# Performance work log

Hardware: AMD Instinct MI355X
Metric: run time of the kernel (lower is better)

Reference implementation:

```python
import jax, jax.numpy as jnp
import numpy as np

B, S, D, H = 4, 2048, 2048, 16
DK = D // H

def setup_inputs() -> dict:
    key = jax.random.key(0)
    ks = jax.random.split(key, 9)
    def xavier(k, shape):
        fan_in, fan_out = shape[1], shape[0]
        limit = (6.0 / (fan_in + fan_out)) ** 0.5
        return jax.random.uniform(k, shape, jnp.float32, -limit, limit)
    return {
        "x": jax.random.normal(ks[0], (B, S, D), jnp.float32),
        "Wq": xavier(ks[1], (D, D)), "bq": jnp.zeros((D,), jnp.float32),
        "Wk": xavier(ks[2], (D, D)), "bk": jnp.zeros((D,), jnp.float32),
        "Wv": xavier(ks[3], (D, D)), "bv": jnp.zeros((D,), jnp.float32),
        "Wo": xavier(ks[4], (D, D)), "bo": jnp.zeros((D,), jnp.float32),
    }

def reference(x, Wq, bq, Wk, bk, Wv, bv, Wo, bo):
    b, s, d = x.shape
    scale = DK ** 0.5
    # torch nn.Linear: y = x @ W.T + b
    def proj(W, bias):
        y = jnp.einsum('bsd,ed->bse', x, W) + bias
        return y.reshape(b, s, H, DK).transpose(0, 2, 1, 3)  # (b, h, s, dk)
    Q, K, V = proj(Wq, bq), proj(Wk, bk), proj(Wv, bv)
    scores = jnp.einsum('bhqd,bhkd->bhqk', Q, K) / scale
    causal = jnp.triu(jnp.ones((s, s), dtype=bool), k=1)
    scores = jnp.where(causal[None, None], -jnp.inf, scores)
    attn = jax.nn.softmax(scores, axis=-1)
    ctx = jnp.einsum('bhqk,bhkd->bhqd', attn, V)
    ctx = ctx.transpose(0, 2, 1, 3).reshape(b, s, d)
    out = jnp.einsum('bsd,ed->bse', ctx, Wo) + bo
    return out
```

## Files before the change

kernel.cpp:

```cpp
#include <hip/hip_runtime.h>
#include <hip/hip_bf16.h>
#include <cstdint>

#define B_  4
#define S_  2048
#define D_  2048
#define H_  16
#define DK_ 128

typedef __attribute__((ext_vector_type(8))) short short8;
typedef __attribute__((ext_vector_type(4))) short s16x4;
typedef __attribute__((ext_vector_type(4))) float f32x4;
typedef unsigned short ushort_t;

__device__ __forceinline__ void gl_lds16(const void* g, void* l) {
  __builtin_amdgcn_global_load_lds(
      (const __attribute__((address_space(1))) uint32_t*)g,
      (__attribute__((address_space(3))) uint32_t*)l, 16, 0, 0);
}

__device__ __forceinline__ ushort_t f2bf(float f) {
  __hip_bfloat16 h = __float2bfloat16(f);
  return *(ushort_t*)&h;
}

__global__ __launch_bounds__(256) void cvt_all(
    const float* __restrict__ x,  const float* __restrict__ w0,
    const float* __restrict__ w1, const float* __restrict__ w2,
    const float* __restrict__ w3, ushort_t* __restrict__ dst)
{
  constexpr size_t NE = (size_t)B_ * S_ * D_;
  constexpr size_t NW = (size_t)D_ * D_;
  constexpr int XB = (int)(NE / 8 / 256);
  constexpr int WB = (int)(NW / 8 / 256);

  const int blk = blockIdx.x;
  const float* src;
  size_t base;
  int li;
  if (blk < XB)           { src = x;  base = 0;           li = blk * 256 + threadIdx.x; }
  else if (blk < XB+WB)   { src = w0; base = NE/8;        li = (blk-XB)     * 256 + threadIdx.x; }
  else if (blk < XB+2*WB) { src = w1; base = (NE+NW)/8;   li = (blk-XB-WB)  * 256 + threadIdx.x; }
  else if (blk < XB+3*WB) { src = w2; base = (NE+2*NW)/8; li = (blk-XB-2*WB)* 256 + threadIdx.x; }
  else                    { src = w3; base = (NE+3*NW)/8; li = (blk-XB-3*WB)* 256 + threadIdx.x; }

  float4 a = ((const float4*)src)[li * 2];
  float4 b = ((const float4*)src)[li * 2 + 1];
  short8 o;
  o[0] = (short)f2bf(a.x); o[1] = (short)f2bf(a.y);
  o[2] = (short)f2bf(a.z); o[3] = (short)f2bf(a.w);
  o[4] = (short)f2bf(b.x); o[5] = (short)f2bf(b.y);
  o[6] = (short)f2bf(b.z); o[7] = (short)f2bf(b.w);
  ((short8*)dst)[base + li] = o;
}

#define STAGE_A(d, q, tt) do {                                             \
    int r0_ = (q) * 64 + w * 8;                                            \
    gl_lds16(Agb + (size_t)(r0_ + lr) * 2048 + (tt) * 64 + lc, &As[d][r0_ * 64]); \
    r0_ += 128;                                                            \
    gl_lds16(Agb + (size_t)(r0_ + lr) * 2048 + (tt) * 64 + lc, &As[d][r0_ * 64]); \
  } while (0)
#define STAGE_B(d, q, tt) do {                                             \
    int r0_ = (w >> 1) * 64 + (q) * 32 + ((w & 1) * 2) * 8;                \
    gl_lds16(Wgb + (size_t)(r0_ + lr) * 2048 + (tt) * 64 + lc, &Bs[d][r0_ * 64]); \
    r0_ += 8;                                                              \
    gl_lds16(Wgb + (size_t)(r0_ + lr) * 2048 + (tt) * 64 + lc, &Bs[d][r0_ * 64]); \
  } while (0)

#define LDA_Q(d, qm) do {                                                  \
    _Pragma("unroll")                                                      \
    for (int fm = 0; fm < 4; ++fm)                                         \
      _Pragma("unroll")                                                    \
      for (int kk = 0; kk < 2; ++kk) {                                     \
        const int row = wm * 128 + (qm) * 64 + fm * 16 + l15;              \
        aA[fm][kk] = *(const short8*)&As[d][row * 64 + (((kk * 4 + lhi) ^ (l15 & 7)) << 3)]; \
      }                                                                    \
  } while (0)

#define LDB_Q(d, bi, qn) do {                                              \
    _Pragma("unroll")                                                      \
    for (int fn = 0; fn < 2; ++fn)                                         \
      _Pragma("unroll")                                                    \
      for (int kk = 0; kk < 2; ++kk) {                                     \
        const int row = wn * 64 + (qn) * 32 + fn * 16 + l15;               \
        bB[bi][fn][kk] = *(const short8*)&Bs[d][row * 64 + (((kk * 4 + lhi) ^ (l15 & 7)) << 3)]; \
      }                                                                    \
  } while (0)

#define MM_Q(am, bi) do {                                                  \
    __builtin_amdgcn_s_setprio(1);                                         \
    _Pragma("unroll")                                                      \
    for (int kk = 0; kk < 2; ++kk)                                         \
      _Pragma("unroll")                                                    \
      for (int fm = 0; fm < 4; ++fm)                                       \
        _Pragma("unroll")                                                  \
        for (int fn = 0; fn < 2; ++fn)                                     \
          acc[(am) * 4 + fm][(bi) * 2 + fn] = __builtin_amdgcn_mfma_f32_16x16x32_bf16( \
              aA[fm][kk], bB[bi][fn][kk], acc[(am) * 4 + fm][(bi) * 2 + fn], 0, 0, 0); \
    __builtin_amdgcn_s_setprio(0);                                         \
  } while (0)

#define GEMM_BODY()                                                        \
  f32x4 acc[8][4] = {};                                                    \
  short8 aA[4][2];                                                         \
  short8 bB[2][2][2];                                                      \
        \
  STAGE_A(0, 0, 0); STAGE_B(0, 0, 0); STAGE_B(0, 1, 0); STAGE_A(0, 1, 0);  \
  STAGE_A(1, 0, 1); STAGE_B(1, 0, 1); STAGE_B(1, 1, 1);                    \
  asm volatile("s_waitcnt vmcnt(6)" ::: "memory");                         \
  __builtin_amdgcn_s_barrier();                                            \
  for (int j = 0; j < NJ; ++j) {                                           \
    const int u = 2 * j;                                                   \
    const bool stg = (j + 1 < NJ);                                         \
                      \
    LDA_Q(0, 0); LDB_Q(0, 0, 0);                                           \
    STAGE_A(1, 1, u + 1);                                                  \
    __builtin_amdgcn_s_barrier();                                          \
    MM_Q(0, 0);                                                            \
    __builtin_amdgcn_s_barrier();                                          \
                                            \
    LDB_Q(0, 1, 1);                                                        \
    if (stg) STAGE_A(0, 0, u + 2);                                         \
    __builtin_amdgcn_s_barrier();                                          \
    MM_Q(0, 1);                                                            \
    __builtin_amdgcn_s_barrier();                                          \
                                            \
    LDA_Q(0, 1);                                                           \
    if (stg) STAGE_B(0, 0, u + 2);                                         \
    __builtin_amdgcn_s_barrier();                                          \
    MM_Q(1, 0);                                                            \
    __builtin_amdgcn_s_barrier();                                          \
                                            \
    if (stg) STAGE_B(0, 1, u + 2);                                         \
    __builtin_amdgcn_s_barrier();                                          \
    MM_Q(1, 1);                                                            \
    if (stg) { asm volatile("s_waitcnt vmcnt(6)" ::: "memory"); }          \
    else     { asm volatile("s_waitcnt vmcnt(0)" ::: "memory"); }          \
    __builtin_amdgcn_s_barrier();                                          \
                                \
    LDA_Q(1, 0); LDB_Q(1, 0, 0);                                           \
    if (stg) STAGE_A(0, 1, u + 2);                                         \
    __builtin_amdgcn_s_barrier();                                          \
    MM_Q(0, 0);                                                            \
    __builtin_amdgcn_s_barrier();                                          \
                                            \
    LDB_Q(1, 1, 1);                                                        \
    if (stg) STAGE_A(1, 0, u + 3);                                         \
    __builtin_amdgcn_s_barrier();                                          \
    MM_Q(0, 1);                                                            \
    __builtin_amdgcn_s_barrier();                                          \
                                            \
    LDA_Q(1, 1);                                                           \
    if (stg) STAGE_B(1, 0, u + 3);                                         \
    __builtin_amdgcn_s_barrier();                                          \
    MM_Q(1, 0);                                                            \
    __builtin_amdgcn_s_barrier();                                          \
                                            \
    if (stg) STAGE_B(1, 1, u + 3);                                         \
    __builtin_amdgcn_s_barrier();                                          \
    MM_Q(1, 1);                                                            \
    if (stg) { asm volatile("s_waitcnt vmcnt(6)" ::: "memory"); }          \
    __builtin_amdgcn_s_barrier();                                          \
  }

__global__ __launch_bounds__(512, 2) void gemmQKV(
    const ushort_t* __restrict__ A,
    const ushort_t* __restrict__ Wqm, const ushort_t* __restrict__ Wkm,
    const ushort_t* __restrict__ Wvm,
    const float* __restrict__ bq, const float* __restrict__ bk,
    const float* __restrict__ bv,
    ushort_t* __restrict__ Qo, ushort_t* __restrict__ Ko,
    ushort_t* __restrict__ Vo)
{
  constexpr int NJ = (D_ / 64) / 2;

  __shared__ ushort_t As[2][256 * 64];
  __shared__ ushort_t Bs[2][256 * 64];

  const int bid = blockIdx.x;
  const int c = bid & 7;
  const int j0 = bid >> 3;
  const int proj = j0 >> 5;
  const int s = j0 & 31;
  const int tnl = s & 7;
  const int tm = c * 4 + (s >> 3);

  const ushort_t* Wsel = (proj == 0) ? Wqm : (proj == 1) ? Wkm : Wvm;
  const float*    bsel = (proj == 0) ? bq  : (proj == 1) ? bk  : bv;
  ushort_t*       osel = (proj == 0) ? Qo  : (proj == 1) ? Ko  : Vo;

  const int t = threadIdx.x;
  const int l = t & 63;
  const int w = t >> 6;
  const int wm = w >> 2;
  const int wn = w & 3;
  const int l15 = l & 15, lhi = l >> 4;
  const int lr = l >> 3;
  const int lc = ((l & 7) ^ lr) * 8;

  const ushort_t* Agb = A + (size_t)(tm * 256) * 2048;
  const ushort_t* Wgb = Wsel + (size_t)(tnl * 256) * 2048;

  GEMM_BODY()

#pragma unroll
  for (int qn = 0; qn < 2; ++qn)
#pragma unroll
    for (int fn = 0; fn < 2; ++fn) {
      const int e = tnl * 256 + wn * 64 + qn * 32 + fn * 16 + l15;
      const float bvv = bsel[e];
      const int h = e >> 7, dk = e & (DK_ - 1);
#pragma unroll
      for (int qm = 0; qm < 2; ++qm)
#pragma unroll
        for (int fm = 0; fm < 4; ++fm) {
          const int srow0 = tm * 256 + wm * 128 + qm * 64 + fm * 16 + lhi * 4;
          const f32x4 v4 = acc[qm * 4 + fm][qn * 2 + fn];
          if (proj == 2) {
            const int b = srow0 >> 11, s0 = srow0 & (S_ - 1);
            s16x4 pk;
#pragma unroll
            for (int r = 0; r < 4; ++r) pk[r] = (short)f2bf(v4[r] + bvv);
            *(s16x4*)(osel + (((size_t)b * H_ + h) * DK_ + dk) * S_ + s0) = pk;
          } else {
#pragma unroll
            for (int r = 0; r < 4; ++r) {
              const int sg = srow0 + r;
              const int b = sg >> 11, sR = sg & (S_ - 1);
              osel[(((size_t)b * H_ + h) * S_ + sR) * DK_ + dk] = f2bf(v4[r] + bvv);
            }
          }
        }
    }
}

__global__ __launch_bounds__(512, 2) void gemmOut(
    const ushort_t* __restrict__ A,
    const ushort_t* __restrict__ W,
    const float* __restrict__ bias,
    float* __restrict__ outp)
{
  constexpr int NJ = (D_ / 64) / 2;
  constexpr int NWG = (B_ * S_ / 256) * (D_ / 256);

  __shared__ ushort_t As[2][256 * 64];
  __shared__ ushort_t Bs[2][256 * 64];

  const int bid = blockIdx.x;
  const int swz = (bid & 7) * (NWG / 8) + (bid >> 3);
  const int tm = swz >> 3;
  const int tn = swz & 7;

  const int t = threadIdx.x;
  const int l = t & 63;
  const int w = t >> 6;
  const int wm = w >> 2;
  const int wn = w & 3;
  const int l15 = l & 15, lhi = l >> 4;
  const int lr = l >> 3;
  const int lc = ((l & 7) ^ lr) * 8;

  const ushort_t* Agb = A + (size_t)(tm * 256) * 2048;
  const ushort_t* Wgb = W + (size_t)(tn * 256) * 2048;

  GEMM_BODY()

#pragma unroll
  for (int qn = 0; qn < 2; ++qn)
#pragma unroll
    for (int fn = 0; fn < 2; ++fn) {
      const int e = tn * 256 + wn * 64 + qn * 32 + fn * 16 + l15;
      const float bvv = bias[e];
#pragma unroll
      for (int qm = 0; qm < 2; ++qm)
#pragma unroll
        for (int fm = 0; fm < 4; ++fm) {
          const int srow0 = tm * 256 + wm * 128 + qm * 64 + fm * 16 + lhi * 4;
          const f32x4 v4 = acc[qm * 4 + fm][qn * 2 + fn];
#pragma unroll
          for (int r = 0; r < 4; ++r)
            outp[(size_t)(srow0 + r) * D_ + e] = v4[r] + bvv;
        }
    }
}
#undef STAGE_A
#undef STAGE_B
#undef LDA_Q
#undef LDB_Q
#undef MM_Q
#undef GEMM_BODY

__global__ __launch_bounds__(256, 2) void attn_kern(
    const ushort_t* __restrict__ Q,
    const ushort_t* __restrict__ K,
    const ushort_t* __restrict__ Vt,
    ushort_t* __restrict__ C)
{
  __shared__ ushort_t Ks[2][64 * 128];
  __shared__ ushort_t Vs[2][128 * 64];
  __shared__ ushort_t Pl[4][32 * 64];

  const int bid = blockIdx.x;
  const int i = bid >> 3;
  const int bh = (bid & 7) * 8 + (i >> 3);
  const int qp = i & 7;

  const ushort_t* Qg = Q + (size_t)bh * S_ * DK_;
  const ushort_t* Kg = K + (size_t)bh * S_ * DK_;
  const ushort_t* Vg = Vt + (size_t)bh * DK_ * S_;
  const int b = bh >> 4, h = bh & 15;

  const int t = threadIdx.x;
  const int l = t & 63;
  const int w = t >> 6;
  const int l15 = l & 15, lhi = l >> 4;

  const float cs = 0.08838834764831845f * 1.4426950408889634f;
  const float DEFER_RAW = 8.0f / cs;

  short8 ones;
#pragma unroll
  for (int j = 0; j < 8; ++j) ones[j] = (short)0x3F80;

  int koff[4], voff[4];
#pragma unroll
  for (int j = 0; j < 4; ++j) {
    const int krow = w * 16 + j * 4 + lhi;
    koff[j] = krow * DK_ + 8 * (l15 ^ ((j * 4 + lhi) & 7));
    const int vrow = (w * 4 + j) * 8 + (l >> 3);
    voff[j] = vrow * S_ + 8 * ((l & 7) ^ (l >> 3));
  }
  int kcol[4];
#pragma unroll
  for (int kt = 0; kt < 4; ++kt)
    kcol[kt] = ((kt * 64 + lhi * 16) ^ ((l15 & 7) << 4)) >> 1;
  int vcol[2];
#pragma unroll
  for (int hb = 0; hb < 2; ++hb)
    vcol[hb] = ((hb * 64 + lhi * 16) ^ ((l15 & 7) << 4)) >> 1;

#define STAGE_KV(pb, kvv) do {                                              \
    _Pragma("unroll")                                                       \
    for (int j = 0; j < 4; ++j) {                                           \
      gl_lds16(Kg + (size_t)(kvv) * DK_ + koff[j], Ks[pb] + (w * 4 + j) * 512); \
      gl_lds16(Vg + (size_t)(kvv) + voff[j],       Vs[pb] + (w * 4 + j) * 512); \
    }                                                                       \
  } while (0)

  for (int pass = 0; pass < 2; ++pass) {
    const int qb = pass ? (15 - qp) : qp;
    const int qrow0 = qb * 128 + w * 32;
    const int nkv = 2 * (qb + 1);

    short8 qa[2][4];
#pragma unroll
    for (int rf = 0; rf < 2; ++rf)
#pragma unroll
      for (int kt = 0; kt < 4; ++kt)
        qa[rf][kt] = *(const short8*)(Qg + (size_t)(qrow0 + rf * 16 + l15) * DK_ + kt * 32 + lhi * 8);

    f32x4 o[2][8] = {};
    f32x4 lsum[2] = {};
    float mrow[2][4];
#pragma unroll
    for (int rf = 0; rf < 2; ++rf)
#pragma unroll
      for (int r = 0; r < 4; ++r) mrow[rf][r] = -1e30f;

    STAGE_KV(0, 0);
    asm volatile("s_waitcnt vmcnt(0)" ::: "memory");
    __syncthreads();

    for (int kvt = 0; kvt < nkv; ++kvt) {
      const int kv = kvt * 64;
      const int p = kvt & 1;

      if (kvt + 1 < nkv) STAGE_KV(p ^ 1, kv + 64);

      f32x4 sf[2][4] = {};
      __builtin_amdgcn_s_setprio(1);
#pragma unroll
      for (int f = 0; f < 4; ++f) {
#pragma unroll
        for (int kt = 0; kt < 4; ++kt) {
          short8 kb = *(const short8*)(Ks[p] + (f * 16 + l15) * 128 + kcol[kt]);
          sf[0][f] = __builtin_amdgcn_mfma_f32_16x16x32_bf16(qa[0][kt], kb, sf[0][f], 0, 0, 0);
          sf[1][f] = __builtin_amdgcn_mfma_f32_16x16x32_bf16(qa[1][kt], kb, sf[1][f], 0, 0, 0);
        }
      }
      __builtin_amdgcn_s_setprio(0);

      float pmax[2][4];
#pragma unroll
      for (int rf = 0; rf < 2; ++rf)
#pragma unroll
        for (int r = 0; r < 4; ++r) pmax[rf][r] = -1e30f;
      const bool domask = (kv + 63 > qrow0);
      if (domask) {
#pragma unroll
        for (int f = 0; f < 4; ++f) {
          const int col = kv + f * 16 + l15;
#pragma unroll
          for (int rf = 0; rf < 2; ++rf)
#pragma unroll
            for (int r = 0; r < 4; ++r) {
              const int row = qrow0 + rf * 16 + lhi * 4 + r;
              if (col > row) sf[rf][f][r] = -1e30f;
              pmax[rf][r] = fmaxf(pmax[rf][r], sf[rf][f][r]);
            }
        }
      } else {
#pragma unroll
        for (int f = 0; f < 4; ++f)
#pragma unroll
          for (int rf = 0; rf < 2; ++rf)
#pragma unroll
            for (int r = 0; r < 4; ++r)
              pmax[rf][r] = fmaxf(pmax[rf][r], sf[rf][f][r]);
      }
#pragma unroll
      for (int d = 1; d < 16; d <<= 1)
#pragma unroll
        for (int rf = 0; rf < 2; ++rf)
#pragma unroll
          for (int r = 0; r < 4; ++r)
            pmax[rf][r] = fmaxf(pmax[rf][r], __shfl_xor(pmax[rf][r], d, 64));

      bool need = false;
#pragma unroll
      for (int rf = 0; rf < 2; ++rf)
#pragma unroll
        for (int r = 0; r < 4; ++r) need |= (pmax[rf][r] > mrow[rf][r] + DEFER_RAW);
      if (__any(need)) {
#pragma unroll
        for (int rf = 0; rf < 2; ++rf)
#pragma unroll
          for (int r = 0; r < 4; ++r) {
            const float mn = fmaxf(mrow[rf][r], pmax[rf][r]);
            const float alpha = __builtin_amdgcn_exp2f((mrow[rf][r] - mn) * cs);
            mrow[rf][r] = mn;
            lsum[rf][r] *= alpha;
#pragma unroll
            for (int n = 0; n < 8; ++n) o[rf][n][r] *= alpha;
          }
      }

      ushort_t* P = Pl[w];
#pragma unroll
      for (int f = 0; f < 4; ++f)
#pragma unroll
        for (int rf = 0; rf < 2; ++rf)
#pragma unroll
          for (int r = 0; r < 4; ++r) {
            const float pv = __builtin_amdgcn_exp2f((sf[rf][f][r] - mrow[rf][r]) * cs);
            const int prow = rf * 16 + lhi * 4 + r;
            P[prow * 64 + ((f * 16 + l15) ^ ((prow & 7) << 3))] = f2bf(pv);
          }

      asm volatile("s_waitcnt lgkmcnt(0)" ::: "memory");
      short8 pa[2][2];
#pragma unroll
      for (int rf = 0; rf < 2; ++rf)
#pragma unroll
        for (int ks = 0; ks < 2; ++ks) {
          const int prow = rf * 16 + l15;
          pa[rf][ks] = *(const short8*)(P + prow * 64 + ((ks * 32 + lhi * 8) ^ ((prow & 7) << 3)));
        }

      __builtin_amdgcn_s_setprio(1);
#pragma unroll
      for (int rf = 0; rf < 2; ++rf) {
        lsum[rf] = __builtin_amdgcn_mfma_f32_16x16x32_bf16(pa[rf][0], ones, lsum[rf], 0, 0, 0);
        lsum[rf] = __builtin_amdgcn_mfma_f32_16x16x32_bf16(pa[rf][1], ones, lsum[rf], 0, 0, 0);
      }
#pragma unroll
      for (int n = 0; n < 8; ++n) {
#pragma unroll
        for (int hb = 0; hb < 2; ++hb) {
          short8 vb = *(const short8*)(Vs[p] + (n * 16 + l15) * 64 + vcol[hb]);
          o[0][n] = __builtin_amdgcn_mfma_f32_16x16x32_bf16(pa[0][hb], vb, o[0][n], 0, 0, 0);
          o[1][n] = __builtin_amdgcn_mfma_f32_16x16x32_bf16(pa[1][hb], vb, o[1][n], 0, 0, 0);
        }
      }
      __builtin_amdgcn_s_setprio(0);

      asm volatile("s_waitcnt vmcnt(0)" ::: "memory");
      __syncthreads();
    }

#pragma unroll
    for (int rf = 0; rf < 2; ++rf) {
      float linv[4];
#pragma unroll
      for (int r = 0; r < 4; ++r) linv[r] = 1.0f / lsum[rf][r];
#pragma unroll
      for (int n = 0; n < 8; ++n) {
        const int dk = n * 16 + l15;
#pragma unroll
        for (int r = 0; r < 4; ++r) {
          const int srow = qrow0 + rf * 16 + lhi * 4 + r;
          C[(((size_t)b * S_ + srow) * H_ + h) * DK_ + dk] = f2bf(o[rf][n][r] * linv[r]);
        }
      }
    }
  }
#undef STAGE_KV
}

extern "C" void kernel_launch(void* const* d_in, const int* in_sizes, int n_in,
                              void* d_out, int out_size, void* d_ws, size_t ws_size,
                              hipStream_t stream) {
  const float* x  = (const float*)d_in[0];
  const float* Wq = (const float*)d_in[1];
  const float* bq = (const float*)d_in[2];
  const float* Wk = (const float*)d_in[3];
  const float* bk = (const float*)d_in[4];
  const float* Wv = (const float*)d_in[5];
  const float* bv = (const float*)d_in[6];
  const float* Wo = (const float*)d_in[7];
  const float* bo = (const float*)d_in[8];
  float* out = (float*)d_out;

  ushort_t* ws = (ushort_t*)d_ws;
  const size_t NE = (size_t)B_ * S_ * D_;
  const size_t NW = (size_t)D_ * D_;
  ushort_t* xb  = ws;
  ushort_t* Wqb = ws + NE;
  ushort_t* Wkb = Wqb + NW;
  ushort_t* Wvb = Wkb + NW;
  ushort_t* Wob = Wvb + NW;
  ushort_t* Qw  = Wob + NW;
  ushort_t* Kw  = Qw + NE;
  ushort_t* Vw  = Kw + NE;
  ushort_t* Cw  = xb;

  const int XB = (int)(NE / 8 / 256);
  const int WB = (int)(NW / 8 / 256);
  cvt_all<<<dim3(XB + 4 * WB), dim3(256), 0, stream>>>(x, Wq, Wk, Wv, Wo, ws);

  gemmQKV<<<dim3(768), dim3(512), 0, stream>>>(xb, Wqb, Wkb, Wvb, bq, bk, bv, Qw, Kw, Vw);
  attn_kern<<<dim3(512), dim3(256), 0, stream>>>(Qw, Kw, Vw, Cw);
  gemmOut<<<dim3(256), dim3(512), 0, stream>>>(Cw, Wob, bo, out);
}
```

Baseline: 449.2 us.

## Switch GEMM mainloop to single LDS buffer with in-place quadrant staging

Replaces the double-buffered LDS pipeline in both projection GEMMs with one 256x64 buffer per operand. The next k-tile is streamed into each quadrant of the buffer as soon as the current tile's fragments for that quadrant have been read into registers, and the number of barriers per k-tile is halved. Setprio is widened to cover the LDS fragment reads as well as the MFMAs. This halves LDS use per block, which may raise occupancy, but it leaves less prefetch distance, so global-load latency is more exposed and the schedule depends on fine-grained waitcnt correctness.

```diff
diff --git a/kernel.cpp b/kernel.cpp
--- a/kernel.cpp
+++ b/kernel.cpp
@@ -54,41 +54,40 @@
   ((short8*)dst)[base + li] = o;
 }
 
-#define STAGE_A(d, q, tt) do {                                             \
+#define STAGE_A(q, tt) do {                                                \
     int r0_ = (q) * 64 + w * 8;                                            \
-    gl_lds16(Agb + (size_t)(r0_ + lr) * 2048 + (tt) * 64 + lc, &As[d][r0_ * 64]); \
+    gl_lds16(Agb + (size_t)(r0_ + lr) * 2048 + (tt) * 64 + lc, &As[r0_ * 64]); \
     r0_ += 128;                                                            \
-    gl_lds16(Agb + (size_t)(r0_ + lr) * 2048 + (tt) * 64 + lc, &As[d][r0_ * 64]); \
+    gl_lds16(Agb + (size_t)(r0_ + lr) * 2048 + (tt) * 64 + lc, &As[r0_ * 64]); \
   } while (0)
-#define STAGE_B(d, q, tt) do {                                             \
+#define STAGE_B(q, tt) do {                                                \
     int r0_ = (w >> 1) * 64 + (q) * 32 + ((w & 1) * 2) * 8;                \
-    gl_lds16(Wgb + (size_t)(r0_ + lr) * 2048 + (tt) * 64 + lc, &Bs[d][r0_ * 64]); \
+    gl_lds16(Wgb + (size_t)(r0_ + lr) * 2048 + (tt) * 64 + lc, &Bs[r0_ * 64]); \
     r0_ += 8;                                                              \
-    gl_lds16(Wgb + (size_t)(r0_ + lr) * 2048 + (tt) * 64 + lc, &Bs[d][r0_ * 64]); \
+    gl_lds16(Wgb + (size_t)(r0_ + lr) * 2048 + (tt) * 64 + lc, &Bs[r0_ * 64]); \
   } while (0)
 
-#define LDA_Q(d, qm) do {                                                  \
+#define LDA_Q(qm) do {                                                     \
     _Pragma("unroll")                                                      \
     for (int fm = 0; fm < 4; ++fm)                                         \
       _Pragma("unroll")                                                    \
       for (int kk = 0; kk < 2; ++kk) {                                     \
         const int row = wm * 128 + (qm) * 64 + fm * 16 + l15;              \
-        aA[fm][kk] = *(const short8*)&As[d][row * 64 + (((kk * 4 + lhi) ^ (l15 & 7)) << 3)]; \
+        aA[fm][kk] = *(const short8*)&As[row * 64 + (((kk * 4 + lhi) ^ (l15 & 7)) << 3)]; \
       }                                                                    \
   } while (0)
 
-#define LDB_Q(d, bi, qn) do {                                              \
+#define LDB_Q(bi, qn) do {                                                 \
     _Pragma("unroll")                                                      \
     for (int fn = 0; fn < 2; ++fn)                                         \
       _Pragma("unroll")                                                    \
       for (int kk = 0; kk < 2; ++kk) {                                     \
         const int row = wn * 64 + (qn) * 32 + fn * 16 + l15;               \
-        bB[bi][fn][kk] = *(const short8*)&Bs[d][row * 64 + (((kk * 4 + lhi) ^ (l15 & 7)) << 3)]; \
+        bB[bi][fn][kk] = *(const short8*)&Bs[row * 64 + (((kk * 4 + lhi) ^ (l15 & 7)) << 3)]; \
       }                                                                    \
   } while (0)
 
 #define MM_Q(am, bi) do {                                                  \
-    __builtin_amdgcn_s_setprio(1);                                         \
     _Pragma("unroll")                                                      \
     for (int kk = 0; kk < 2; ++kk)                                         \
       _Pragma("unroll")                                                    \
@@ -97,69 +96,48 @@
         for (int fn = 0; fn < 2; ++fn)                                     \
           acc[(am) * 4 + fm][(bi) * 2 + fn] = __builtin_amdgcn_mfma_f32_16x16x32_bf16( \
               aA[fm][kk], bB[bi][fn][kk], acc[(am) * 4 + fm][(bi) * 2 + fn], 0, 0, 0); \
-    __builtin_amdgcn_s_setprio(0);                                         \
   } while (0)
 
 #define GEMM_BODY()                                                        \
   f32x4 acc[8][4] = {};                                                    \
   short8 aA[4][2];                                                         \
   short8 bB[2][2][2];                                                      \
-        \
-  STAGE_A(0, 0, 0); STAGE_B(0, 0, 0); STAGE_B(0, 1, 0); STAGE_A(0, 1, 0);  \
-  STAGE_A(1, 0, 1); STAGE_B(1, 0, 1); STAGE_B(1, 1, 1);                    \
-  asm volatile("s_waitcnt vmcnt(6)" ::: "memory");                         \
+  STAGE_A(0, 0); STAGE_A(1, 0); STAGE_B(0, 0); STAGE_B(1, 0);              \
+  asm volatile("s_waitcnt vmcnt(0)" ::: "memory");                         \
   __builtin_amdgcn_s_barrier();                                            \
-  for (int j = 0; j < NJ; ++j) {                                           \
-    const int u = 2 * j;                                                   \
-    const bool stg = (j + 1 < NJ);                                         \
-                      \
-    LDA_Q(0, 0); LDB_Q(0, 0, 0);                                           \
-    STAGE_A(1, 1, u + 1);                                                  \
+  for (int kt = 0; kt < NT; ++kt) {                                        \
+    const bool stg = (kt + 1 < NT);                                        \
+       \
+    __builtin_amdgcn_s_setprio(1);                                         \
+    LDA_Q(0); LDB_Q(0, 0);                                                 \
+    MM_Q(0, 0);                                                            \
+    __builtin_amdgcn_s_setprio(0);                                         \
+    asm volatile("s_waitcnt vmcnt(2) lgkmcnt(0)" ::: "memory");            \
     __builtin_amdgcn_s_barrier();                                          \
-    MM_Q(0, 0);                                                            \
+            \
+    if (stg) { STAGE_A(0, kt + 1); STAGE_B(0, kt + 1); }                   \
+    __builtin_amdgcn_s_setprio(1);                                         \
+    LDB_Q(1, 1);                                                           \
+    MM_Q(0, 1);                                                            \
+    __builtin_amdgcn_s_setprio(0);                                         \
+    if (stg) { asm volatile("s_waitcnt vmcnt(4) lgkmcnt(0)" ::: "memory"); } \
+    else     { asm volatile("s_waitcnt vmcnt(0) lgkmcnt(0)" ::: "memory"); } \
     __builtin_amdgcn_s_barrier();                                          \
-                                            \
-    LDB_Q(0, 1, 1);                                                        \
-    if (stg) STAGE_A(0, 0, u + 2);                                         \
+               \
+    if (stg) STAGE_B(1, kt + 1);                                           \
+    __builtin_amdgcn_s_setprio(1);                                         \
+    LDA_Q(1);                                                              \
+    MM_Q(1, 0);                                                            \
+    __builtin_amdgcn_s_setprio(0);                                         \
+    asm volatile("s_waitcnt lgkmcnt(0)" ::: "memory");                     \
     __builtin_amdgcn_s_barrier();                                          \
-    MM_Q(0, 1);                                                            \
-    __builtin_amdgcn_s_barrier();                                          \
-                                            \
-    LDA_Q(0, 1);                                                           \
-    if (stg) STAGE_B(0, 0, u + 2);                                         \
-    __builtin_amdgcn_s_barrier();                                          \
-    MM_Q(1, 0);                                                            \
-    __builtin_amdgcn_s_barrier();                                          \
-                                            \
-    if (stg) STAGE_B(0, 1, u + 2);                                         \
-    __builtin_amdgcn_s_barrier();                                          \
+                             \
+    if (stg) STAGE_A(1, kt + 1);                                           \
+    __builtin_amdgcn_s_setprio(1);                                         \
     MM_Q(1, 1);                                                            \
-    if (stg) { asm volatile("s_waitcnt vmcnt(6)" ::: "memory"); }          \
+    __builtin_amdgcn_s_setprio(0);                                         \
+    if (stg) { asm volatile("s_waitcnt vmcnt(4)" ::: "memory"); }          \
     else     { asm volatile("s_waitcnt vmcnt(0)" ::: "memory"); }          \
-    __builtin_amdgcn_s_barrier();                                          \
-                                \
-    LDA_Q(1, 0); LDB_Q(1, 0, 0);                                           \
-    if (stg) STAGE_A(0, 1, u + 2);                                         \
-    __builtin_amdgcn_s_barrier();                                          \
-    MM_Q(0, 0);                                                            \
-    __builtin_amdgcn_s_barrier();                                          \
-                                            \
-    LDB_Q(1, 1, 1);                                                        \
-    if (stg) STAGE_A(1, 0, u + 3);                                         \
-    __builtin_amdgcn_s_barrier();                                          \
-    MM_Q(0, 1);                                                            \
-    __builtin_amdgcn_s_barrier();                                          \
-                                            \
-    LDA_Q(1, 1);                                                           \
-    if (stg) STAGE_B(1, 0, u + 3);                                         \
-    __builtin_amdgcn_s_barrier();                                          \
-    MM_Q(1, 0);                                                            \
-    __builtin_amdgcn_s_barrier();                                          \
-                                            \
-    if (stg) STAGE_B(1, 1, u + 3);                                         \
-    __builtin_amdgcn_s_barrier();                                          \
-    MM_Q(1, 1);                                                            \
-    if (stg) { asm volatile("s_waitcnt vmcnt(6)" ::: "memory"); }          \
     __builtin_amdgcn_s_barrier();                                          \
   }
 
@@ -172,10 +150,10 @@
     ushort_t* __restrict__ Qo, ushort_t* __restrict__ Ko,
     ushort_t* __restrict__ Vo)
 {
-  constexpr int NJ = (D_ / 64) / 2;
-
-  __shared__ ushort_t As[2][256 * 64];
-  __shared__ ushort_t Bs[2][256 * 64];
+  constexpr int NT = D_ / 64;
+
+  __shared__ ushort_t As[256 * 64];
+  __shared__ ushort_t Bs[256 * 64];
 
   const int bid = blockIdx.x;
   const int c = bid & 7;
@@ -240,11 +218,11 @@
     const float* __restrict__ bias,
     float* __restrict__ outp)
 {
-  constexpr int NJ = (D_ / 64) / 2;
+  constexpr int NT = D_ / 64;
   constexpr int NWG = (B_ * S_ / 256) * (D_ / 256);
 
-  __shared__ ushort_t As[2][256 * 64];
-  __shared__ ushort_t Bs[2][256 * 64];
+  __shared__ ushort_t As[256 * 64];
+  __shared__ ushort_t Bs[256 * 64];
 
   const int bid = blockIdx.x;
   const int swz = (bid & 7) * (NWG / 8) + (bid >> 3);
```

Result: slower. 481.6 us (+7.2%).
